# Performance work log

Measured on AMD Instinct MI355X. Metric: run time of the kernel, lower is better.

Reference implementation:

```python
import jax, jax.numpy as jnp
import numpy as np

B, E, LC, LE, D = 32, 8, 256, 512, 256   # batch, evi_num, claim_len, evidence_len, emb_dim
OUT, H = 128, 1                          # attention hidden dim, head_num
NEG = -1e18


def setup_inputs() -> dict:
    key = jax.random.key(0)
    ks = jax.random.split(key, 8)
    claim = jax.random.normal(ks[0], (B, E, LC, D), jnp.float32)
    evidence = jax.random.normal(ks[1], (B, E, LE, D), jnp.float32)
    claim_len_mask = jax.random.randint(ks[2], (B, E, 1, LC), 0, 2).astype(jnp.int32)
    evidence_len_mask = jax.random.randint(ks[3], (B, E, 1, LE), 0, 2).astype(jnp.int32)
    s2d = 1.0 / np.sqrt(2 * D)
    so = 1.0 / np.sqrt(OUT)
    W1 = jax.random.normal(ks[4], (2 * D, OUT), jnp.float32) * s2d  # torch W1.weight.T
    w2 = jax.random.normal(ks[5], (OUT, H), jnp.float32) * so
    W2 = jax.random.normal(ks[6], (2 * D, OUT), jnp.float32) * s2d
    w1 = jax.random.normal(ks[7], (OUT, H), jnp.float32) * so
    return {"claim": claim, "claim_len_mask": claim_len_mask,
            "evidence": evidence, "evidence_len_mask": evidence_len_mask,
            "W1": W1, "w2": w2, "W2": W2, "w1": w1}


def _pooled_attend(seq, seq_mask, pooled, W, w):
    # seq: (B,E,L,D), pooled: (B,E,1,D), W: (2D,OUT), w: (OUT,H)
    # cat([seq, pooled_expanded]) @ W  ==  seq @ W[:D] + pooled @ W[D:]  (broadcast)
    h = jnp.tanh(seq @ W[:D] + pooled @ W[D:])          # (B,E,L,OUT)
    att = h @ w                                          # (B,E,L,H)
    mask = jnp.swapaxes(seq_mask, -1, -2).astype(bool)   # (B,E,L,1), broadcast over H
    att = jnp.where(mask, att, NEG)
    scores = jax.nn.softmax(att, axis=-2)                # softmax over L
    out = jnp.einsum('belh,beld->behd', scores, seq)     # (B,E,H,D)
    return out.reshape(out.shape[0], out.shape[1], 1, -1)  # (B,E,1,H*D)


def reference(claim, claim_len_mask, evidence, evidence_len_mask, W1, w2, W2, w1):
    c_mean = jnp.mean(claim, axis=-2, keepdims=True)     # (B,E,1,D)
    e_hat = _pooled_attend(evidence, evidence_len_mask, c_mean, W1, w2)
    e_mean = jnp.mean(evidence, axis=-2, keepdims=True)  # (B,E,1,D)
    c_hat = _pooled_attend(claim, claim_len_mask, e_mean, W2, w1)
    return c_hat, e_hat
```

## Files before the change

### kernel.cpp

```cpp
#include <hip/hip_runtime.h>
#include <hip/hip_bf16.h>
#include <math.h>

#define BE   256
#define DIM  256
#define OUTD 128
#define LCL  256
#define LEV  512
#define NEGV -1e18f

typedef short  bf16x8  __attribute__((ext_vector_type(8)));
typedef float  floatx4 __attribute__((ext_vector_type(4)));

union BF1 { __hip_bfloat16 h; unsigned short u; };
union BF2 { __hip_bfloat162 h; unsigned int u; };

__device__ __forceinline__ float fast_tanh(float x) {
    float xc = fminf(fmaxf(x, -15.f), 15.f);
    float e = __expf(2.f * xc);
    return (e - 1.f) * __builtin_amdgcn_rcpf(e + 1.f);
}

__device__ __forceinline__ void gl_lds16(const float4* g, float4* l) {
    __builtin_amdgcn_global_load_lds(
        (const __attribute__((address_space(1))) unsigned int*)(const void*)g,
        (__attribute__((address_space(3))) unsigned int*)(void*)l,
        16, 0, 0);
}

__global__ __launch_bounds__(512) void k_meanbias(
    const float* __restrict__ claim, const float* __restrict__ evidence,
    const float* __restrict__ W1, const float* __restrict__ W2,
    float* __restrict__ bias_e, float* __restrict__ bias_c,
    unsigned short* __restrict__ WT1, unsigned short* __restrict__ WT2)
{
    const int bid = blockIdx.x;
    const int t = threadIdx.x;
    if (bid >= BE) {
        const int side = bid - BE;
        const float* W = side ? W2 : W1;
        unsigned short* WT = side ? WT2 : WT1;
        for (int i = t; i < OUTD * DIM; i += 512) {
            const int d = i & (DIM - 1);
            const int n = i >> 8;
            BF1 c; c.h = __float2bfloat16(W[(size_t)d * OUTD + n]);
            WT[n * DIM + d] = c.u;
        }
        return;
    }
    const int pair = bid;
    const int d4 = t & 63, rg = t >> 6;
    __shared__ float4 smc[8][64];
    __shared__ float4 sme[8][64];
    __shared__ float mc[DIM], me[DIM];
    __shared__ float sb[2][2][OUTD];

    const float4* c4 = (const float4*)(claim + (size_t)pair * LCL * DIM);
    const float4* e4 = (const float4*)(evidence + (size_t)pair * LEV * DIM);
    float4 ac = make_float4(0.f, 0.f, 0.f, 0.f);
    float4 ae = make_float4(0.f, 0.f, 0.f, 0.f);
#pragma unroll 8
    for (int r = rg; r < LCL; r += 8) {
        const float4 v = c4[r * 64 + d4];
        ac.x += v.x; ac.y += v.y; ac.z += v.z; ac.w += v.w;
    }
#pragma unroll 8
    for (int r = rg; r < LEV; r += 8) {
        const float4 v = e4[r * 64 + d4];
        ae.x += v.x; ae.y += v.y; ae.z += v.z; ae.w += v.w;
    }
    smc[rg][d4] = ac; sme[rg][d4] = ae;
    __syncthreads();
    if (t < 64) {
        float4 s = make_float4(0.f, 0.f, 0.f, 0.f);
#pragma unroll
        for (int j = 0; j < 8; ++j) {
            const float4 v = smc[j][t];
            s.x += v.x; s.y += v.y; s.z += v.z; s.w += v.w;
        }
        ((float4*)mc)[t] = make_float4(s.x * (1.f / LCL), s.y * (1.f / LCL),
                                       s.z * (1.f / LCL), s.w * (1.f / LCL));
    } else if (t < 128) {
        const int u = t - 64;
        float4 s = make_float4(0.f, 0.f, 0.f, 0.f);
#pragma unroll
        for (int j = 0; j < 8; ++j) {
            const float4 v = sme[j][u];
            s.x += v.x; s.y += v.y; s.z += v.z; s.w += v.w;
        }
        ((float4*)me)[u] = make_float4(s.x * (1.f / LEV), s.y * (1.f / LEV),
                                       s.z * (1.f / LEV), s.w * (1.f / LEV));
    }
    __syncthreads();
    const int side = t >> 8, o = t & 127, dh = (t >> 7) & 1;
    const float* W = side ? W2 : W1;
    const float* m = side ? me : mc;
    float s = 0.f;
#pragma unroll 8
    for (int i = 0; i < 128; ++i) {
        const int d = dh * 128 + i;
        s += m[d] * W[(size_t)(DIM + d) * OUTD + o];
    }
    sb[side][dh][o] = s;
    __syncthreads();
    if (t < 256) {
        const int sd = t >> 7, oo = t & 127;
        const float bv = sb[sd][0][oo] + sb[sd][1][oo];
        (sd ? bias_c : bias_e)[pair * OUTD + oo] = bv;
    }
}

__global__ __launch_bounds__(512, 2) void k_fused(
    const float* __restrict__ claim, const float* __restrict__ evidence,
    const unsigned short* __restrict__ WT1, const unsigned short* __restrict__ WT2,
    const float* __restrict__ w2v, const float* __restrict__ w1v,
    const float* __restrict__ bias_e, const float* __restrict__ bias_c,
    const int* __restrict__ emask, const int* __restrict__ cmask,
    float* __restrict__ out)
{
    constexpr int TR  = 32;
    constexpr int SR4 = 65;
    __shared__ float4 sA4[2][TR * SR4];
    __shared__ float sred[TR][4];

    const int bid = blockIdx.x;
    const bool is_ev = (bid & 1) == 0;
    const int pair = bid >> 1;
    const float* __restrict__ seq  = is_ev ? evidence : claim;
    const unsigned short* __restrict__ WT = is_ev ? WT1 : WT2;
    const float* __restrict__ wvec = is_ev ? w2v : w1v;
    const float* __restrict__ bias = is_ev ? bias_e : bias_c;
    const int*   __restrict__ mask = is_ev ? emask : cmask;
    float* __restrict__ outp       = is_ev ? out + (size_t)BE * DIM : out;
    const int L  = is_ev ? LEV : LCL;
    const int NT = L >> 5;

    const int t = threadIdx.x;
    const int lane = t & 63;
    const int wv = t >> 6;
    const int wrowf = wv >> 2;
    const int wcg = wv & 3;
    const int q = lane >> 4, c16 = lane & 15;

    float bc[2], wc[2];
#pragma unroll
    for (int ct = 0; ct < 2; ++ct) {
        const int col = wcg * 32 + ct * 16 + c16;
        bc[ct] = bias[pair * OUTD + col];
        wc[ct] = wvec[col];
    }
    const unsigned short* wbase = WT + (size_t)(wcg * 32 + c16) * DIM + q * 8;
    const float4* sp4 = (const float4*)(seq + (size_t)pair * L * DIM);

    auto stage = [&](int buf, int tile) {
        const float4* base = sp4 + (size_t)tile * (TR * 64);
#pragma unroll
        for (int j = 0; j < 4; ++j) {
            const int row = wv * 4 + j;
            gl_lds16(base + row * 64 + lane, &sA4[buf][row * SR4]);
        }
    };

    stage(0, 0);
    int cur = 0;

    float4 Oac = make_float4(0.f, 0.f, 0.f, 0.f);
    float m_run = -INFINITY, l_run = 0.f;

    for (int tile = 0; tile < NT; ++tile) {
        asm volatile("s_waitcnt vmcnt(0) lgkmcnt(0)" ::: "memory");
        __builtin_amdgcn_s_barrier();
        if (tile + 1 < NT) stage(cur ^ 1, tile + 1);

        floatx4 acc[2];
        acc[0] = (floatx4){0.f, 0.f, 0.f, 0.f};
        acc[1] = (floatx4){0.f, 0.f, 0.f, 0.f};
        const int arow = wrowf * 16 + c16;
#pragma unroll
        for (int ks = 0; ks < 8; ++ks) {
            bf16x8 bfr[2];
#pragma unroll
            for (int ct = 0; ct < 2; ++ct)
                bfr[ct] = *(const bf16x8*)(wbase + (size_t)ct * 16 * DIM + ks * 32);
            const float4 lo = sA4[cur][arow * SR4 + ks * 8 + q * 2];
            const float4 hi = sA4[cur][arow * SR4 + ks * 8 + q * 2 + 1];
            union { bf16x8 v; BF2 p[4]; } ua;
            ua.p[0].h = __float22bfloat162_rn(make_float2(lo.x, lo.y));
            ua.p[1].h = __float22bfloat162_rn(make_float2(lo.z, lo.w));
            ua.p[2].h = __float22bfloat162_rn(make_float2(hi.x, hi.y));
            ua.p[3].h = __float22bfloat162_rn(make_float2(hi.z, hi.w));
#pragma unroll
            for (int ct = 0; ct < 2; ++ct)
                acc[ct] = __builtin_amdgcn_mfma_f32_16x16x32_bf16(ua.v, bfr[ct], acc[ct], 0, 0, 0);
        }

#pragma unroll
        for (int reg = 0; reg < 4; ++reg) {
            float s = 0.f;
#pragma unroll
            for (int ct = 0; ct < 2; ++ct)
                s += fast_tanh(acc[ct][reg] + bc[ct]) * wc[ct];
#pragma unroll
            for (int off = 1; off < 16; off <<= 1) s += __shfl_xor(s, off, 64);
            if (c16 == 0)
                sred[wrowf * 16 + q * 4 + reg][wcg] = s;
        }
        asm volatile("s_waitcnt lgkmcnt(0)" ::: "memory");
        __builtin_amdgcn_s_barrier();

        const int row = lane & 31;
        float a = sred[row][0] + sred[row][1] + sred[row][2] + sred[row][3];
        a = mask[pair * L + tile * TR + row] ? a : NEGV;
        float mx = a;
#pragma unroll
        for (int off = 1; off < 64; off <<= 1) mx = fmaxf(mx, __shfl_xor(mx, off, 64));
        const float newm = fmaxf(m_run, mx);
        const float e = __expf(a - newm);
        float sm = e;
#pragma unroll
        for (int off = 1; off < 64; off <<= 1) sm += __shfl_xor(sm, off, 64);
        const float scale = __expf(m_run - newm);
        l_run = l_run * scale + 0.5f * sm;
        m_run = newm;
        Oac.x *= scale; Oac.y *= scale; Oac.z *= scale; Oac.w *= scale;

#pragma unroll
        for (int r = 0; r < 4; ++r) {
            const int rw = wv * 4 + r;
            const float pl = __shfl(e, rw, 64);
            const float4 v = sA4[cur][rw * SR4 + lane];
            Oac.x += pl * v.x; Oac.y += pl * v.y; Oac.z += pl * v.z; Oac.w += pl * v.w;
        }
        cur ^= 1;
    }

    __syncthreads();
    ((float4*)sA4)[t] = Oac;
    __syncthreads();
    if (t < 64) {
        float4 s = make_float4(0.f, 0.f, 0.f, 0.f);
#pragma unroll
        for (int j = 0; j < 8; ++j) {
            const float4 v = ((float4*)sA4)[j * 64 + t];
            s.x += v.x; s.y += v.y; s.z += v.z; s.w += v.w;
        }
        const float inv = 1.f / l_run;
        ((float4*)(outp + (size_t)pair * DIM))[t] =
            make_float4(s.x * inv, s.y * inv, s.z * inv, s.w * inv);
    }
}

extern "C" void kernel_launch(void* const* d_in, const int* in_sizes, int n_in,
                              void* d_out, int out_size, void* d_ws, size_t ws_size,
                              hipStream_t stream) {
    const float* claim    = (const float*)d_in[0];
    const int*   cmask    = (const int*)  d_in[1];
    const float* evidence = (const float*)d_in[2];
    const int*   emask    = (const int*)  d_in[3];
    const float* W1       = (const float*)d_in[4];
    const float* w2       = (const float*)d_in[5];
    const float* W2       = (const float*)d_in[6];
    const float* w1       = (const float*)d_in[7];
    float* out = (float*)d_out;

    float* ws = (float*)d_ws;
    float* bias_e = ws;
    float* bias_c = bias_e + BE * OUTD;
    unsigned short* WT1 = (unsigned short*)(bias_c + BE * OUTD);
    unsigned short* WT2 = WT1 + OUTD * DIM;

    k_meanbias<<<BE + 2, 512, 0, stream>>>(claim, evidence, W1, W2,
                                           bias_e, bias_c, WT1, WT2);
    k_fused<<<2 * BE, 512, 0, stream>>>(claim, evidence, WT1, WT2, w2, w1,
                                        bias_e, bias_c, emask, cmask, out);
}
```

Baseline: 399.9 us.

## Double row tile to 64, keep weight fragments in registers, prefetch mask

Doubles the sequence tile per iteration from 32 to 64 rows. Each wave now computes two 16-row MFMA blocks, which halves the number of barrier-synchronized tile iterations. The bf16 weight fragments are loaded once into 16 registers instead of being reloaded from global memory every tile, and the mask is loaded at the top of each tile. In exchange it doubles LDS usage (about 133KB), lowers launch bounds to one block per CU, and raises register pressure, which reduces occupancy.

```diff
diff --git a/kernel.cpp b/kernel.cpp
--- a/kernel.cpp
+++ b/kernel.cpp
@@ -110,7 +110,7 @@
     }
 }
 
-__global__ __launch_bounds__(512, 2) void k_fused(
+__global__ __launch_bounds__(512, 1) void k_fused(
     const float* __restrict__ claim, const float* __restrict__ evidence,
     const unsigned short* __restrict__ WT1, const unsigned short* __restrict__ WT2,
     const float* __restrict__ w2v, const float* __restrict__ w1v,
@@ -118,10 +118,10 @@
     const int* __restrict__ emask, const int* __restrict__ cmask,
     float* __restrict__ out)
 {
-    constexpr int TR  = 32;
+    constexpr int TR  = 64;
     constexpr int SR4 = 65;
     __shared__ float4 sA4[2][TR * SR4];
-    __shared__ float sred[TR][4];
+    __shared__ float sred[4][TR];
 
     const int bid = blockIdx.x;
     const bool is_ev = (bid & 1) == 0;
@@ -133,7 +133,7 @@
     const int*   __restrict__ mask = is_ev ? emask : cmask;
     float* __restrict__ outp       = is_ev ? out + (size_t)BE * DIM : out;
     const int L  = is_ev ? LEV : LCL;
-    const int NT = L >> 5;
+    const int NT = L >> 6;
 
     const int t = threadIdx.x;
     const int lane = t & 63;
@@ -141,6 +141,7 @@
     const int wrowf = wv >> 2;
     const int wcg = wv & 3;
     const int q = lane >> 4, c16 = lane & 15;
+    const int arowb = wrowf * 32;
 
     float bc[2], wc[2];
 #pragma unroll
@@ -149,14 +150,22 @@
         bc[ct] = bias[pair * OUTD + col];
         wc[ct] = wvec[col];
     }
-    const unsigned short* wbase = WT + (size_t)(wcg * 32 + c16) * DIM + q * 8;
+
+    bf16x8 breg[16];
+#pragma unroll
+    for (int ks = 0; ks < 8; ++ks)
+#pragma unroll
+        for (int ct = 0; ct < 2; ++ct)
+            breg[ks * 2 + ct] = *(const bf16x8*)(
+                WT + (size_t)(wcg * 32 + ct * 16 + c16) * DIM + ks * 32 + q * 8);
+
     const float4* sp4 = (const float4*)(seq + (size_t)pair * L * DIM);
 
     auto stage = [&](int buf, int tile) {
         const float4* base = sp4 + (size_t)tile * (TR * 64);
 #pragma unroll
-        for (int j = 0; j < 4; ++j) {
-            const int row = wv * 4 + j;
+        for (int j = 0; j < 8; ++j) {
+            const int row = wv * 8 + j;
             gl_lds16(base + row * 64 + lane, &sA4[buf][row * SR4]);
         }
     };
@@ -171,46 +180,48 @@
         asm volatile("s_waitcnt vmcnt(0) lgkmcnt(0)" ::: "memory");
         __builtin_amdgcn_s_barrier();
         if (tile + 1 < NT) stage(cur ^ 1, tile + 1);
-
-        floatx4 acc[2];
-        acc[0] = (floatx4){0.f, 0.f, 0.f, 0.f};
-        acc[1] = (floatx4){0.f, 0.f, 0.f, 0.f};
-        const int arow = wrowf * 16 + c16;
+        const int mk = mask[pair * L + tile * TR + lane];
+
+        floatx4 acc[2][2];
+        acc[0][0] = (floatx4){0.f, 0.f, 0.f, 0.f};
+        acc[0][1] = (floatx4){0.f, 0.f, 0.f, 0.f};
+        acc[1][0] = (floatx4){0.f, 0.f, 0.f, 0.f};
+        acc[1][1] = (floatx4){0.f, 0.f, 0.f, 0.f};
 #pragma unroll
         for (int ks = 0; ks < 8; ++ks) {
-            bf16x8 bfr[2];
-#pragma unroll
-            for (int ct = 0; ct < 2; ++ct)
-                bfr[ct] = *(const bf16x8*)(wbase + (size_t)ct * 16 * DIM + ks * 32);
-            const float4 lo = sA4[cur][arow * SR4 + ks * 8 + q * 2];
-            const float4 hi = sA4[cur][arow * SR4 + ks * 8 + q * 2 + 1];
-            union { bf16x8 v; BF2 p[4]; } ua;
-            ua.p[0].h = __float22bfloat162_rn(make_float2(lo.x, lo.y));
-            ua.p[1].h = __float22bfloat162_rn(make_float2(lo.z, lo.w));
-            ua.p[2].h = __float22bfloat162_rn(make_float2(hi.x, hi.y));
-            ua.p[3].h = __float22bfloat162_rn(make_float2(hi.z, hi.w));
-#pragma unroll
-            for (int ct = 0; ct < 2; ++ct)
-                acc[ct] = __builtin_amdgcn_mfma_f32_16x16x32_bf16(ua.v, bfr[ct], acc[ct], 0, 0, 0);
-        }
-
-#pragma unroll
-        for (int reg = 0; reg < 4; ++reg) {
-            float s = 0.f;
-#pragma unroll
-            for (int ct = 0; ct < 2; ++ct)
-                s += fast_tanh(acc[ct][reg] + bc[ct]) * wc[ct];
-#pragma unroll
-            for (int off = 1; off < 16; off <<= 1) s += __shfl_xor(s, off, 64);
-            if (c16 == 0)
-                sred[wrowf * 16 + q * 4 + reg][wcg] = s;
+#pragma unroll
+            for (int ra = 0; ra < 2; ++ra) {
+                const float4 lo = sA4[cur][(arowb + ra * 16 + c16) * SR4 + ks * 8 + q * 2];
+                const float4 hi = sA4[cur][(arowb + ra * 16 + c16) * SR4 + ks * 8 + q * 2 + 1];
+                union { bf16x8 v; BF2 p[4]; } ua;
+                ua.p[0].h = __float22bfloat162_rn(make_float2(lo.x, lo.y));
+                ua.p[1].h = __float22bfloat162_rn(make_float2(lo.z, lo.w));
+                ua.p[2].h = __float22bfloat162_rn(make_float2(hi.x, hi.y));
+                ua.p[3].h = __float22bfloat162_rn(make_float2(hi.z, hi.w));
+#pragma unroll
+                for (int ct = 0; ct < 2; ++ct)
+                    acc[ra][ct] = __builtin_amdgcn_mfma_f32_16x16x32_bf16(
+                        ua.v, breg[ks * 2 + ct], acc[ra][ct], 0, 0, 0);
+            }
+        }
+
+#pragma unroll
+        for (int ra = 0; ra < 2; ++ra) {
+#pragma unroll
+            for (int reg = 0; reg < 4; ++reg) {
+                float s = fast_tanh(acc[ra][0][reg] + bc[0]) * wc[0]
+                        + fast_tanh(acc[ra][1][reg] + bc[1]) * wc[1];
+#pragma unroll
+                for (int off = 1; off < 16; off <<= 1) s += __shfl_xor(s, off, 64);
+                if (c16 == 0)
+                    sred[wcg][arowb + ra * 16 + q * 4 + reg] = s;
+            }
         }
         asm volatile("s_waitcnt lgkmcnt(0)" ::: "memory");
         __builtin_amdgcn_s_barrier();
 
-        const int row = lane & 31;
-        float a = sred[row][0] + sred[row][1] + sred[row][2] + sred[row][3];
-        a = mask[pair * L + tile * TR + row] ? a : NEGV;
+        float a = sred[0][lane] + sred[1][lane] + sred[2][lane] + sred[3][lane];
+        a = mk ? a : NEGV;
         float mx = a;
 #pragma unroll
         for (int off = 1; off < 64; off <<= 1) mx = fmaxf(mx, __shfl_xor(mx, off, 64));
@@ -220,13 +231,13 @@
 #pragma unroll
         for (int off = 1; off < 64; off <<= 1) sm += __shfl_xor(sm, off, 64);
         const float scale = __expf(m_run - newm);
-        l_run = l_run * scale + 0.5f * sm;
+        l_run = l_run * scale + sm;
         m_run = newm;
         Oac.x *= scale; Oac.y *= scale; Oac.z *= scale; Oac.w *= scale;
 
 #pragma unroll
-        for (int r = 0; r < 4; ++r) {
-            const int rw = wv * 4 + r;
+        for (int r = 0; r < 8; ++r) {
+            const int rw = wv * 8 + r;
             const float pl = __shfl(e, rw, 64);
             const float4 v = sA4[cur][rw * SR4 + lane];
             Oac.x += pl * v.x; Oac.y += pl * v.y; Oac.z += pl * v.z; Oac.w += pl * v.w;
```

Result: faster. 370.3 us (-7.4%).
